# Kernel optimization log

Measured on AMD Instinct MI355X. Metric: run time of the kernel, lower is better.

## Reference

```python
import jax, jax.numpy as jnp
import numpy as np

EPS = 1e-5

def _ln(x, g, b):
    mu = x.mean(-1, keepdims=True)
    var = ((x - mu) ** 2).mean(-1, keepdims=True)
    return (x - mu) * jax.lax.rsqrt(var + EPS) * g + b

def setup_inputs() -> dict:
    B, K, D, H, T = 64, 64, 128, 128, 4
    key = jax.random.key(0)
    ks = jax.random.split(key, 20)
    s = 0.02
    inp = {
        "slots": jax.random.normal(ks[0], (B, K, D), jnp.float32),
        "edge_probs": jax.random.uniform(ks[1], (B, K, K), jnp.float32),
        "edge_types": jax.random.uniform(ks[2], (B, K, K, T), jnp.float32),
        # f_self: LayerNorm(D) -> Linear(D,H) -> ReLU -> Linear(H,D)
        "ls_g": jnp.ones((D,), jnp.float32),
        "ls_b": jnp.zeros((D,), jnp.float32),
        "ws1": jax.random.normal(ks[3], (D, H), jnp.float32) * s,
        "bs1": jnp.zeros((H,), jnp.float32),
        "ws2": jax.random.normal(ks[4], (H, D), jnp.float32) * s,
        "bs2": jnp.zeros((D,), jnp.float32),
        # f_inter[tau]: Linear(2D,H) -> ReLU -> Linear(H,H) -> ReLU -> Linear(H,D), stacked over T
        "wi1": jax.random.normal(ks[5], (T, 2 * D, H), jnp.float32) * s,
        "bi1": jnp.zeros((T, H), jnp.float32),
        "wi2": jax.random.normal(ks[6], (T, H, H), jnp.float32) * s,
        "bi2": jnp.zeros((T, H), jnp.float32),
        "wi3": jax.random.normal(ks[7], (T, H, D), jnp.float32) * s,
        "bi3": jnp.zeros((T, D), jnp.float32),
        # update_mlp: LayerNorm(2D) -> Linear(2D,H) -> ReLU -> Linear(H,D)
        "lu_g": jnp.ones((2 * D,), jnp.float32),
        "lu_b": jnp.zeros((2 * D,), jnp.float32),
        "wu1": jax.random.normal(ks[8], (2 * D, H), jnp.float32) * s,
        "bu1": jnp.zeros((H,), jnp.float32),
        "wu2": jax.random.normal(ks[9], (H, D), jnp.float32) * s,
        "bu2": jnp.zeros((D,), jnp.float32),
    }
    return inp

NUM_MP = 2

def reference(slots, edge_probs, edge_types, ls_g, ls_b, ws1, bs1, ws2, bs2,
              wi1, bi1, wi2, bi2, wi3, bi3, lu_g, lu_b, wu1, bu1, wu2, bu2):
    B, K, D = slots.shape
    T = edge_types.shape[-1]
    h = slots
    for _ in range(NUM_MP):
        # f_self
        delta_self = jax.nn.relu(_ln(h, ls_g, ls_b) @ ws1 + bs1) @ ws2 + bs2
        # all-pairs features: cat[b,i,j] = [h[b,i] (sender), h[b,j] (receiver)]
        sender = jnp.broadcast_to(h[:, :, None, :], (B, K, K, D))
        receiver = jnp.broadcast_to(h[:, None, :, :], (B, K, K, D))
        pair = jnp.concatenate([sender, receiver], axis=-1)  # [B,K,K,2D]
        delta_inter = jnp.zeros_like(h)
        for tau in range(T):
            x = jax.nn.relu(pair @ wi1[tau] + bi1[tau])
            x = jax.nn.relu(x @ wi2[tau] + bi2[tau])
            eff = x @ wi3[tau] + bi3[tau]  # [B,K,K,D]
            w = edge_probs[..., None] * edge_types[..., tau, None]  # [B,K,K,1]
            delta_inter = delta_inter + (eff * w).sum(axis=1)  # sum over sender i
        combined = jnp.concatenate([h + delta_self, delta_inter], axis=-1)
        update = jax.nn.relu(_ln(combined, lu_g, lu_b) @ wu1 + bu1) @ wu2 + bu2
        h = h + update  # residual=True
    return h
```

## Files before the change

### kernel.cpp

```cpp
#include <hip/hip_runtime.h>
#include <hip/hip_fp16.h>

#define BATCH 64
#define KSLOT 64
#define DDIM  128
#define HDIM  128
#define TTYPE 4
#define NSLOT (BATCH*KSLOT)
#define EPSLN 1e-5f
#define YROW  544

typedef _Float16 v8h __attribute__((ext_vector_type(8)));
typedef float    v4f __attribute__((ext_vector_type(4)));

__device__ __forceinline__ float waveAllSum(float v) {
    #pragma unroll
    for (int m = 1; m < 64; m <<= 1) v += __shfl_xor(v, m, 64);
    return v;
}

__global__ __launch_bounds__(256) void k_wconv(
        const float* __restrict__ ws1, const float* __restrict__ wi1,
        const float* __restrict__ ws2, const float* __restrict__ wu1,
        const float* __restrict__ wu2, const float* __restrict__ wi3,
        const float* __restrict__ wi2, const float* __restrict__ bi1,
        const float* __restrict__ bi3,
        __half* __restrict__ ws1T, __half* __restrict__ wi1catT,
        __half* __restrict__ ws2T, __half* __restrict__ wu1T,
        __half* __restrict__ wu2T, __half* __restrict__ w3catT,
        __half* __restrict__ w2T16, float* __restrict__ biascat) {
    __shared__ __align__(16) float tile[128*132];
    int bx = blockIdx.x, tid = threadIdx.x;
    if (bx == 21) {
        for (int idx = tid; idx < 128*32; idx += 256) {
            int o = idx >> 5, c = idx & 31;
            w3catT[(size_t)o*YROW + 512 + c] = (c < 4) ? __float2half(bi3[c*DDIM + o]) : __float2half(0.f);
        }
        for (int idx = tid; idx < 1024; idx += 256) {
            int th = idx >> 7, o = idx & 127;
            biascat[idx] = (th & 1) ? bi1[(th>>1)*HDIM + o] : 0.f;
        }
        return;
    }
    const float* src; __half* dst; int dstride = 128, dcol = 0;
    if (bx == 0)      { src = ws1; dst = ws1T; }
    else if (bx <= 8) { int th = bx-1, tau = th>>1, half = th&1;
                        src = wi1 + ((size_t)tau*256 + half*128)*128;
                        dst = wi1catT + (size_t)th*128*128; }
    else if (bx == 9) { src = ws2; dst = ws2T; }
    else if (bx ==10) { src = wu2; dst = wu2T; }
    else if (bx <=12) { int hh = bx-11; src = wu1 + (size_t)hh*128*128;
                        dst = wu1T; dstride = 256; dcol = hh*128; }
    else if (bx <=16) { int tau = bx-13; src = wi3 + (size_t)tau*16384;
                        dst = w3catT; dstride = YROW; dcol = tau*128; }
    else              { int tau = bx-17; src = wi2 + (size_t)tau*16384;
                        dst = w2T16 + (size_t)tau*16384; }
    for (int idx = tid; idx < 4096; idx += 256) {
        int r = idx >> 5, c4 = idx & 31;
        *(float4*)&tile[r*132 + c4*4] = *(const float4*)&src[(size_t)r*128 + c4*4];
    }
    __syncthreads();
    for (int idx = tid; idx < 8192; idx += 256) {
        int n = idx >> 6, kp = idx & 63;
        __half2 p = __floats2half2_rn(tile[(2*kp)*132 + n], tile[(2*kp+1)*132 + n]);
        *(__half2*)&dst[(size_t)n*dstride + dcol + 2*kp] = p;
    }
}

__global__ __launch_bounds__(256) void k_front(
        const float* __restrict__ h,
        const __half* __restrict__ wi1catT, const float* __restrict__ biascat,
        const float* __restrict__ ls_g, const float* __restrict__ ls_b,
        const __half* __restrict__ ws1T, const float* __restrict__ bs1,
        const __half* __restrict__ ws2T, const float* __restrict__ bs2,
        __half* __restrict__ AtCt, float* __restrict__ comb128) {
    __shared__ __align__(16) char smem[17152];
    int tid = threadIdx.x, lane = tid & 63, w = tid >> 6;
    int n = lane & 15, quad = lane >> 4;
    int row0 = blockIdx.x*16, nb = blockIdx.y;
    if (nb < 4) {
        _Float16* Ha = (_Float16*)smem;
        for (int u = tid; u < 16*32; u += 256) {
            int r = u >> 5, c4 = (u & 31)*4;
            float4 f = *(const float4*)&h[(size_t)(row0 + r)*128 + c4];
            *(__half2*)&Ha[r*136 + c4]     = __floats2half2_rn(f.x, f.y);
            *(__half2*)&Ha[r*136 + c4 + 2] = __floats2half2_rn(f.z, f.w);
        }
        __syncthreads();
        v8h bfrag[4][4];
        #pragma unroll
        for (int ot = 0; ot < 4; ot++) {
            int col = nb*256 + w*64 + ot*16 + n;
            #pragma unroll
            for (int ks = 0; ks < 4; ks++)
                bfrag[ot][ks] = *(const v8h*)&wi1catT[(size_t)col*128 + ks*32 + quad*8];
        }
        v4f acc[4];
        #pragma unroll
        for (int ot = 0; ot < 4; ot++) {
            float b0 = biascat[nb*256 + w*64 + ot*16 + n];
            acc[ot] = (v4f){b0, b0, b0, b0};
        }
        #pragma unroll
        for (int ks = 0; ks < 4; ks++) {
            v8h a = *(const v8h*)&Ha[n*136 + ks*32 + quad*8];
            #pragma unroll
            for (int ot = 0; ot < 4; ot++)
                acc[ot] = __builtin_amdgcn_mfma_f32_16x16x32_f16(a, bfrag[ot][ks], acc[ot], 0, 0, 0);
        }
        #pragma unroll
        for (int ot = 0; ot < 4; ot++)
            #pragma unroll
            for (int r = 0; r < 4; r++) {
                int row = row0 + quad*4 + r, col = nb*256 + w*64 + ot*16 + n;
                AtCt[(size_t)row*1024 + col] = __float2half(acc[ot][r]);
            }
    } else {
        float*    Hrow = (float*)smem;
        _Float16* Xa = (_Float16*)(smem + 8448);
        _Float16* Tt = (_Float16*)(smem + 8448 + 4352);
        v8h b1[2][4], b2[2][4];
        #pragma unroll
        for (int ot = 0; ot < 2; ot++) {
            int col = w*32 + ot*16 + n;
            #pragma unroll
            for (int ks = 0; ks < 4; ks++) {
                b1[ot][ks] = *(const v8h*)&ws1T[(size_t)col*128 + ks*32 + quad*8];
                b2[ot][ks] = *(const v8h*)&ws2T[(size_t)col*128 + ks*32 + quad*8];
            }
        }
        for (int u = tid; u < 16*32; u += 256) {
            int r = u >> 5, c4 = (u & 31)*4;
            *(float4*)&Hrow[r*132 + c4] = *(const float4*)&h[(size_t)(row0 + r)*128 + c4];
        }
        __syncthreads();
        #pragma unroll
        for (int rr = 0; rr < 4; rr++) {
            int r = w*4 + rr;
            float x0 = Hrow[r*132 + 2*lane], x1 = Hrow[r*132 + 2*lane + 1];
            float mu = waveAllSum(x0 + x1) * (1.f/128.f);
            float d0 = x0 - mu, d1 = x1 - mu;
            float var = waveAllSum(d0*d0 + d1*d1) * (1.f/128.f);
            float rs = rsqrtf(var + EPSLN);
            float2 gv = *(const float2*)&ls_g[2*lane];
            float2 bv = *(const float2*)&ls_b[2*lane];
            *(__half2*)&Xa[r*136 + 2*lane] = __floats2half2_rn(d0*rs*gv.x + bv.x, d1*rs*gv.y + bv.y);
        }
        __syncthreads();
        v4f acc[2];
        #pragma unroll
        for (int ot = 0; ot < 2; ot++) { float b0 = bs1[w*32 + ot*16 + n]; acc[ot] = (v4f){b0,b0,b0,b0}; }
        #pragma unroll
        for (int ks = 0; ks < 4; ks++) {
            v8h a = *(const v8h*)&Xa[n*136 + ks*32 + quad*8];
            #pragma unroll
            for (int ot = 0; ot < 2; ot++)
                acc[ot] = __builtin_amdgcn_mfma_f32_16x16x32_f16(a, b1[ot][ks], acc[ot], 0, 0, 0);
        }
        #pragma unroll
        for (int ot = 0; ot < 2; ot++)
            #pragma unroll
            for (int r = 0; r < 4; r++)
                Tt[(quad*4 + r)*136 + w*32 + ot*16 + n] = (_Float16)fmaxf(acc[ot][r], 0.f);
        __syncthreads();
        #pragma unroll
        for (int ot = 0; ot < 2; ot++) { float b0 = bs2[w*32 + ot*16 + n]; acc[ot] = (v4f){b0,b0,b0,b0}; }
        #pragma unroll
        for (int ks = 0; ks < 4; ks++) {
            v8h a = *(const v8h*)&Tt[n*136 + ks*32 + quad*8];
            #pragma unroll
            for (int ot = 0; ot < 2; ot++)
                acc[ot] = __builtin_amdgcn_mfma_f32_16x16x32_f16(a, b2[ot][ks], acc[ot], 0, 0, 0);
        }
        #pragma unroll
        for (int ot = 0; ot < 2; ot++)
            #pragma unroll
            for (int r = 0; r < 4; r++) {
                int rr = quad*4 + r, col = w*32 + ot*16 + n;
                comb128[(size_t)(row0 + rr)*128 + col] = Hrow[rr*132 + col] + acc[ot][r];
            }
    }
}

#define LROW 136
__global__ __launch_bounds__(512) void k_pair(
        const __half* __restrict__ AtCt,
        const __half* __restrict__ w2T16,
        const float* __restrict__ bi2,
        const float* __restrict__ ep, const float* __restrict__ et,
        __half* __restrict__ Ycat) {
    __shared__ __align__(16) _Float16 w2T[HDIM*LROW];
    __shared__ __align__(16) _Float16 Cs[KSLOT*LROW];
    __shared__ __align__(16) _Float16 As[KSLOT*LROW];
    __shared__ __align__(16) _Float16 wS[KSLOT*KSLOT];
    int bx = blockIdx.x, b = bx >> 2, tau = bx & 3;
    int tid = threadIdx.x, lane = tid & 63, w = tid >> 6;
    int jt = w >> 1, oh = w & 1, quad = lane >> 4, n = lane & 15;

    for (int idx = tid; idx < 2048; idx += 512) {
        int o = idx >> 4, seg = (idx & 15)*8;
        *(v8h*)&w2T[o*LROW + seg] = *(const v8h*)&w2T16[((size_t)tau*128 + o)*128 + seg];
    }
    for (int u = tid; u < 1024; u += 512) {
        int j = u >> 4, seg = (u & 15)*8;
        const __half* rp = AtCt + (size_t)(b*KSLOT + j)*1024 + tau*256 + seg;
        *(v8h*)&As[j*LROW + seg] = *(const v8h*)&rp[0];
        *(v8h*)&Cs[j*LROW + seg] = *(const v8h*)&rp[128];
    }
    {
        const float* epb = ep + (size_t)b*KSLOT*KSLOT;
        const float* etb = et + (size_t)b*KSLOT*KSLOT*TTYPE + tau;
        for (int idx = tid; idx < KSLOT*KSLOT; idx += 512)
            wS[idx] = (_Float16)(epb[idx] * etb[(size_t)idx*TTYPE]);
    }
    __syncthreads();

    v8h bfrag[4][4];
    #pragma unroll
    for (int ot = 0; ot < 4; ot++)
        #pragma unroll
        for (int ks = 0; ks < 4; ks++)
            bfrag[ot][ks] = *(const v8h*)&w2T[(oh*64 + ot*16 + n)*LROW + ks*32 + quad*8];
    v8h cfrag[4];
    #pragma unroll
    for (int ks = 0; ks < 4; ks++)
        cfrag[ks] = *(const v8h*)&Cs[(jt*16 + n)*LROW + ks*32 + quad*8];
    float biasv[4];
    #pragma unroll
    for (int ot = 0; ot < 4; ot++) biasv[ot] = bi2[tau*HDIM + oh*64 + ot*16 + n];

    v4f yacc[4];
    #pragma unroll
    for (int ot = 0; ot < 4; ot++) yacc[ot] = (v4f){0.f,0.f,0.f,0.f};
    float wsacc[4] = {0.f,0.f,0.f,0.f};
    const v8h zero8 = {0,0,0,0,0,0,0,0};

    for (int i = 0; i < KSLOT; ++i) {
        v8h x1[4];
        #pragma unroll
        for (int ks = 0; ks < 4; ks++) {
            v8h a = *(const v8h*)&As[i*LROW + ks*32 + quad*8];
            x1[ks] = __builtin_elementwise_max(a + cfrag[ks], zero8);
        }
        _Float16 wv16[4];
        #pragma unroll
        for (int r = 0; r < 4; r++) wv16[r] = wS[i*KSLOT + jt*16 + quad*4 + r];
        #pragma unroll
        for (int ot = 0; ot < 4; ot++) {
            v4f acc = (v4f){biasv[ot], biasv[ot], biasv[ot], biasv[ot]};
            #pragma unroll
            for (int ks = 0; ks < 4; ks++)
                acc = __builtin_amdgcn_mfma_f32_16x16x32_f16(x1[ks], bfrag[ot][ks], acc, 0, 0, 0);
            #pragma unroll
            for (int r = 0; r < 4; r++)
                yacc[ot][r] = fmaf((float)wv16[r], fmaxf(acc[r], 0.f), yacc[ot][r]);
        }
        #pragma unroll
        for (int r = 0; r < 4; r++) wsacc[r] += (float)wv16[r];
    }

    #pragma unroll
    for (int r = 0; r < 4; r++) {
        int j = jt*16 + quad*4 + r;
        __half* yb = Ycat + (size_t)(b*KSLOT + j)*YROW + tau*128 + oh*64;
        #pragma unroll
        for (int ot = 0; ot < 4; ot++)
            yb[ot*16 + n] = __float2half(yacc[ot][r]);
    }
    if (oh == 0 && n == 0) {
        #pragma unroll
        for (int r = 0; r < 4; r++)
            Ycat[(size_t)(b*KSLOT + jt*16 + quad*4 + r)*YROW + 512 + tau] = __float2half(wsacc[r]);
    }
}

__global__ __launch_bounds__(256) void k_mega(
        const __half* __restrict__ Ycat, const __half* __restrict__ w3catT,
        const float* __restrict__ comb128,
        const float* __restrict__ g, const float* __restrict__ bb,
        const __half* __restrict__ wu1T, const float* __restrict__ bu1,
        const __half* __restrict__ wu2T, const float* __restrict__ bu2,
        const float* __restrict__ h, float* __restrict__ hout) {
    __shared__ __align__(16) _Float16 Ys[16*552];
    __shared__ __align__(16) float    Crow[16*260];
    __shared__ __align__(16) _Float16 Xa[16*264];
    __shared__ __align__(16) _Float16 Ut[16*136];
    int tid = threadIdx.x, lane = tid & 63, w = tid >> 6;
    int n = lane & 15, quad = lane >> 4;
    int row0 = blockIdx.x*16;
    for (int u = tid; u < 1024; u += 256) {
        int r = u >> 6, seg = (u & 63)*8;
        *(v8h*)&Ys[r*552 + seg] = *(const v8h*)&Ycat[(size_t)(row0 + r)*YROW + seg];
    }
    {
        int r = tid >> 2, seg = 512 + (tid & 3)*8;
        if (tid < 64) *(v8h*)&Ys[r*552 + seg] = *(const v8h*)&Ycat[(size_t)(row0 + r)*YROW + seg];
    }
    for (int u = tid; u < 16*32; u += 256) {
        int r = u >> 5, c4 = (u & 31)*4;
        *(float4*)&Crow[r*260 + c4] = *(const float4*)&comb128[(size_t)(row0 + r)*128 + c4];
    }
    __syncthreads();
    {
        v4f acc[2];
        acc[0] = (v4f){0.f,0.f,0.f,0.f};
        acc[1] = (v4f){0.f,0.f,0.f,0.f};
        #pragma unroll
        for (int ks = 0; ks < 17; ks++) {
            v8h a = *(const v8h*)&Ys[n*552 + ks*32 + quad*8];
            #pragma unroll
            for (int o2 = 0; o2 < 2; o2++) {
                v8h bfr = *(const v8h*)&w3catT[(size_t)(w*32 + o2*16 + n)*YROW + ks*32 + quad*8];
                acc[o2] = __builtin_amdgcn_mfma_f32_16x16x32_f16(a, bfr, acc[o2], 0, 0, 0);
            }
        }
        #pragma unroll
        for (int o2 = 0; o2 < 2; o2++)
            #pragma unroll
            for (int r = 0; r < 4; r++)
                Crow[(quad*4 + r)*260 + 128 + w*32 + o2*16 + n] = acc[o2][r];
    }
    __syncthreads();
    #pragma unroll
    for (int rr = 0; rr < 4; rr++) {
        int r = w*4 + rr;
        float4 v = *(const float4*)&Crow[r*260 + 4*lane];
        float mu = waveAllSum(v.x + v.y + v.z + v.w) * (1.f/256.f);
        float d0 = v.x-mu, d1 = v.y-mu, d2 = v.z-mu, d3 = v.w-mu;
        float var = waveAllSum(d0*d0 + d1*d1 + d2*d2 + d3*d3) * (1.f/256.f);
        float rs = rsqrtf(var + EPSLN);
        float4 gv = *(const float4*)&g[4*lane];
        float4 bv = *(const float4*)&bb[4*lane];
        *(__half2*)&Xa[r*264 + 4*lane]     = __floats2half2_rn(d0*rs*gv.x + bv.x, d1*rs*gv.y + bv.y);
        *(__half2*)&Xa[r*264 + 4*lane + 2] = __floats2half2_rn(d2*rs*gv.z + bv.z, d3*rs*gv.w + bv.w);
    }
    __syncthreads();
    v4f acc[2];
    #pragma unroll
    for (int ot = 0; ot < 2; ot++) { float b0 = bu1[w*32 + ot*16 + n]; acc[ot] = (v4f){b0,b0,b0,b0}; }
    #pragma unroll
    for (int ks = 0; ks < 8; ks++) {
        v8h a = *(const v8h*)&Xa[n*264 + ks*32 + quad*8];
        #pragma unroll
        for (int ot = 0; ot < 2; ot++) {
            v8h bfr = *(const v8h*)&wu1T[(size_t)(w*32 + ot*16 + n)*256 + ks*32 + quad*8];
            acc[ot] = __builtin_amdgcn_mfma_f32_16x16x32_f16(a, bfr, acc[ot], 0, 0, 0);
        }
    }
    #pragma unroll
    for (int ot = 0; ot < 2; ot++)
        #pragma unroll
        for (int r = 0; r < 4; r++)
            Ut[(quad*4 + r)*136 + w*32 + ot*16 + n] = (_Float16)fmaxf(acc[ot][r], 0.f);
    __syncthreads();
    #pragma unroll
    for (int ot = 0; ot < 2; ot++) { float b0 = bu2[w*32 + ot*16 + n]; acc[ot] = (v4f){b0,b0,b0,b0}; }
    #pragma unroll
    for (int ks = 0; ks < 4; ks++) {
        v8h a = *(const v8h*)&Ut[n*136 + ks*32 + quad*8];
        #pragma unroll
        for (int ot = 0; ot < 2; ot++) {
            v8h bfr = *(const v8h*)&wu2T[(size_t)(w*32 + ot*16 + n)*128 + ks*32 + quad*8];
            acc[ot] = __builtin_amdgcn_mfma_f32_16x16x32_f16(a, bfr, acc[ot], 0, 0, 0);
        }
    }
    #pragma unroll
    for (int ot = 0; ot < 2; ot++)
        #pragma unroll
        for (int r = 0; r < 4; r++) {
            int rr = quad*4 + r, col = w*32 + ot*16 + n;
            hout[(size_t)(row0 + rr)*128 + col] = h[(size_t)(row0 + rr)*128 + col] + acc[ot][r];
        }
}

extern "C" void kernel_launch(void* const* d_in, const int* in_sizes, int n_in,
                              void* d_out, int out_size, void* d_ws, size_t ws_size,
                              hipStream_t stream) {
    const float* slots = (const float*)d_in[0];
    const float* ep    = (const float*)d_in[1];
    const float* et    = (const float*)d_in[2];
    const float* ls_g  = (const float*)d_in[3];
    const float* ls_b  = (const float*)d_in[4];
    const float* ws1   = (const float*)d_in[5];
    const float* bs1   = (const float*)d_in[6];
    const float* ws2   = (const float*)d_in[7];
    const float* bs2   = (const float*)d_in[8];
    const float* wi1   = (const float*)d_in[9];
    const float* bi1   = (const float*)d_in[10];
    const float* wi2   = (const float*)d_in[11];
    const float* bi2   = (const float*)d_in[12];
    const float* wi3   = (const float*)d_in[13];
    const float* bi3   = (const float*)d_in[14];
    const float* lu_g  = (const float*)d_in[15];
    const float* lu_b  = (const float*)d_in[16];
    const float* wu1   = (const float*)d_in[17];
    const float* bu1   = (const float*)d_in[18];
    const float* wu2   = (const float*)d_in[19];
    const float* bu2   = (const float*)d_in[20];
    float* out = (float*)d_out;

    char* p = (char*)d_ws;
    float*  h_buf   = (float*)p;   p += (size_t)NSLOT*DDIM*4;
    __half* AtCt    = (__half*)p;  p += (size_t)NSLOT*1024*2;
    __half* Ycat    = (__half*)p;  p += (size_t)NSLOT*YROW*2;
    float*  comb128 = (float*)p;   p += (size_t)NSLOT*128*4;
    __half* ws1T    = (__half*)p;  p += 128*128*2;
    __half* wi1catT = (__half*)p;  p += 1024*128*2;
    __half* ws2T    = (__half*)p;  p += 128*128*2;
    __half* wu1T    = (__half*)p;  p += 128*256*2;
    __half* wu2T    = (__half*)p;  p += 128*128*2;
    __half* w3catT  = (__half*)p;  p += 128*YROW*2;
    __half* w2T16   = (__half*)p;  p += 4*128*128*2;
    float*  biascat = (float*)p;   p += 1024*4;

    k_wconv<<<22, 256, 0, stream>>>(ws1, wi1, ws2, wu1, wu2, wi3, wi2, bi1, bi3,
                                    ws1T, wi1catT, ws2T, wu1T, wu2T, w3catT, w2T16, biascat);

    for (int mp = 0; mp < 2; mp++) {
        const float* h = (mp == 0) ? slots : h_buf;
        float* hout = (mp == 0) ? h_buf : out;
        k_front<<<dim3(256, 5), 256, 0, stream>>>(h, wi1catT, biascat, ls_g, ls_b,
                                                  ws1T, bs1, ws2T, bs2, AtCt, comb128);
        k_pair<<<BATCH*TTYPE, 512, 0, stream>>>(AtCt, w2T16, bi2, ep, et, Ycat);
        k_mega<<<NSLOT/16, 256, 0, stream>>>(Ycat, w3catT, comb128, lu_g, lu_b,
                                             wu1T, bu1, wu2T, bu2, h, hout);
    }
}
```

Baseline: 229.3 us.

## Double wave count in pair and mega kernels, prefetch next sender row

k_pair now runs 1024 threads per block, with each wave owning 32 output columns instead of 64. This halves the per-wave B fragments and accumulators, and the inner loop software-prefetches the next sender row and edge weights from LDS. k_mega moves to 512 threads, each wave producing 16 output columns, so more waves hide the global weight loads. The trade is more redundant A-operand LDS reads and x1 recomputation per block. Occupancy is also limited by the 1024-thread blocks and LDS use.

New measurement: 252.2 us. 1.1x slower.

```diff
diff --git a/kernel.cpp b/kernel.cpp
--- a/kernel.cpp
+++ b/kernel.cpp
@@ -11,6 +11,7 @@
 #define YROW  544
 
 typedef _Float16 v8h __attribute__((ext_vector_type(8)));
+typedef _Float16 v4h __attribute__((ext_vector_type(4)));
 typedef float    v4f __attribute__((ext_vector_type(4)));
 
 __device__ __forceinline__ float waveAllSum(float v) {
@@ -183,7 +184,7 @@
 }
 
 #define LROW 136
-__global__ __launch_bounds__(512) void k_pair(
+__global__ __launch_bounds__(1024, 4) void k_pair(
         const __half* __restrict__ AtCt,
         const __half* __restrict__ w2T16,
         const float* __restrict__ bi2,
@@ -195,14 +196,14 @@
     __shared__ __align__(16) _Float16 wS[KSLOT*KSLOT];
     int bx = blockIdx.x, b = bx >> 2, tau = bx & 3;
     int tid = threadIdx.x, lane = tid & 63, w = tid >> 6;
-    int jt = w >> 1, oh = w & 1, quad = lane >> 4, n = lane & 15;
-
-    for (int idx = tid; idx < 2048; idx += 512) {
+    int jt = w >> 2, oq = w & 3, quad = lane >> 4, n = lane & 15;
+
+    for (int idx = tid; idx < 2048; idx += 1024) {
         int o = idx >> 4, seg = (idx & 15)*8;
         *(v8h*)&w2T[o*LROW + seg] = *(const v8h*)&w2T16[((size_t)tau*128 + o)*128 + seg];
     }
-    for (int u = tid; u < 1024; u += 512) {
-        int j = u >> 4, seg = (u & 15)*8;
+    {
+        int j = tid >> 4, seg = (tid & 15)*8;
         const __half* rp = AtCt + (size_t)(b*KSLOT + j)*1024 + tau*256 + seg;
         *(v8h*)&As[j*LROW + seg] = *(const v8h*)&rp[0];
         *(v8h*)&Cs[j*LROW + seg] = *(const v8h*)&rp[128];
@@ -210,71 +211,80 @@
     {
         const float* epb = ep + (size_t)b*KSLOT*KSLOT;
         const float* etb = et + (size_t)b*KSLOT*KSLOT*TTYPE + tau;
-        for (int idx = tid; idx < KSLOT*KSLOT; idx += 512)
+        for (int idx = tid; idx < KSLOT*KSLOT; idx += 1024)
             wS[idx] = (_Float16)(epb[idx] * etb[(size_t)idx*TTYPE]);
     }
     __syncthreads();
 
-    v8h bfrag[4][4];
-    #pragma unroll
-    for (int ot = 0; ot < 4; ot++)
+    v8h bfrag[2][4];
+    #pragma unroll
+    for (int ot = 0; ot < 2; ot++)
         #pragma unroll
         for (int ks = 0; ks < 4; ks++)
-            bfrag[ot][ks] = *(const v8h*)&w2T[(oh*64 + ot*16 + n)*LROW + ks*32 + quad*8];
+            bfrag[ot][ks] = *(const v8h*)&w2T[(oq*32 + ot*16 + n)*LROW + ks*32 + quad*8];
     v8h cfrag[4];
     #pragma unroll
     for (int ks = 0; ks < 4; ks++)
         cfrag[ks] = *(const v8h*)&Cs[(jt*16 + n)*LROW + ks*32 + quad*8];
-    float biasv[4];
-    #pragma unroll
-    for (int ot = 0; ot < 4; ot++) biasv[ot] = bi2[tau*HDIM + oh*64 + ot*16 + n];
-
-    v4f yacc[4];
-    #pragma unroll
-    for (int ot = 0; ot < 4; ot++) yacc[ot] = (v4f){0.f,0.f,0.f,0.f};
+    float biasv[2];
+    #pragma unroll
+    for (int ot = 0; ot < 2; ot++) biasv[ot] = bi2[tau*HDIM + oq*32 + ot*16 + n];
+
+    v4f yacc[2];
+    yacc[0] = (v4f){0.f,0.f,0.f,0.f};
+    yacc[1] = (v4f){0.f,0.f,0.f,0.f};
     float wsacc[4] = {0.f,0.f,0.f,0.f};
     const v8h zero8 = {0,0,0,0,0,0,0,0};
 
+    v8h aN[4]; v4h wvN;
+    #pragma unroll
+    for (int ks = 0; ks < 4; ks++) aN[ks] = *(const v8h*)&As[ks*32 + quad*8];
+    wvN = *(const v4h*)&wS[jt*16 + quad*4];
+
     for (int i = 0; i < KSLOT; ++i) {
+        v8h a[4]; v4h wv = wvN;
+        #pragma unroll
+        for (int ks = 0; ks < 4; ks++) a[ks] = aN[ks];
+        if (i < KSLOT-1) {
+            #pragma unroll
+            for (int ks = 0; ks < 4; ks++)
+                aN[ks] = *(const v8h*)&As[(i+1)*LROW + ks*32 + quad*8];
+            wvN = *(const v4h*)&wS[(i+1)*KSLOT + jt*16 + quad*4];
+        }
         v8h x1[4];
         #pragma unroll
-        for (int ks = 0; ks < 4; ks++) {
-            v8h a = *(const v8h*)&As[i*LROW + ks*32 + quad*8];
-            x1[ks] = __builtin_elementwise_max(a + cfrag[ks], zero8);
-        }
-        _Float16 wv16[4];
-        #pragma unroll
-        for (int r = 0; r < 4; r++) wv16[r] = wS[i*KSLOT + jt*16 + quad*4 + r];
-        #pragma unroll
-        for (int ot = 0; ot < 4; ot++) {
+        for (int ks = 0; ks < 4; ks++)
+            x1[ks] = __builtin_elementwise_max(a[ks] + cfrag[ks], zero8);
+        #pragma unroll
+        for (int ot = 0; ot < 2; ot++) {
             v4f acc = (v4f){biasv[ot], biasv[ot], biasv[ot], biasv[ot]};
             #pragma unroll
             for (int ks = 0; ks < 4; ks++)
                 acc = __builtin_amdgcn_mfma_f32_16x16x32_f16(x1[ks], bfrag[ot][ks], acc, 0, 0, 0);
             #pragma unroll
             for (int r = 0; r < 4; r++)
-                yacc[ot][r] = fmaf((float)wv16[r], fmaxf(acc[r], 0.f), yacc[ot][r]);
-        }
-        #pragma unroll
-        for (int r = 0; r < 4; r++) wsacc[r] += (float)wv16[r];
+                yacc[ot][r] = fmaf((float)wv[r], fmaxf(acc[r], 0.f), yacc[ot][r]);
+        }
+        #pragma unroll
+        for (int r = 0; r < 4; r++) wsacc[r] += (float)wv[r];
     }
 
     #pragma unroll
     for (int r = 0; r < 4; r++) {
         int j = jt*16 + quad*4 + r;
-        __half* yb = Ycat + (size_t)(b*KSLOT + j)*YROW + tau*128 + oh*64;
-        #pragma unroll
-        for (int ot = 0; ot < 4; ot++)
+        __half* yb = Ycat + (size_t)(b*KSLOT + j)*YROW + tau*128 + oq*32;
+        #pragma unroll
+        for (int ot = 0; ot < 2; ot++)
             yb[ot*16 + n] = __float2half(yacc[ot][r]);
     }
-    if (oh == 0 && n == 0) {
+    if (oq == 0 && n == 0) {
         #pragma unroll
         for (int r = 0; r < 4; r++)
             Ycat[(size_t)(b*KSLOT + jt*16 + quad*4 + r)*YROW + 512 + tau] = __float2half(wsacc[r]);
     }
 }
 
-__global__ __launch_bounds__(256) void k_mega(
+__global__ __launch_bounds__(512) void k_mega(
         const __half* __restrict__ Ycat, const __half* __restrict__ w3catT,
         const float* __restrict__ comb128,
         const float* __restrict__ g, const float* __restrict__ bb,
@@ -288,42 +298,35 @@
     int tid = threadIdx.x, lane = tid & 63, w = tid >> 6;
     int n = lane & 15, quad = lane >> 4;
     int row0 = blockIdx.x*16;
-    for (int u = tid; u < 1024; u += 256) {
+    for (int u = tid; u < 1024; u += 512) {
         int r = u >> 6, seg = (u & 63)*8;
         *(v8h*)&Ys[r*552 + seg] = *(const v8h*)&Ycat[(size_t)(row0 + r)*YROW + seg];
     }
+    if (tid < 64) {
+        int r = tid >> 2, seg = 512 + (tid & 3)*8;
+        *(v8h*)&Ys[r*552 + seg] = *(const v8h*)&Ycat[(size_t)(row0 + r)*YROW + seg];
+    }
+    if (tid < 512) {
+        int r = tid >> 5, c4 = (tid & 31)*4;
+        *(float4*)&Crow[r*260 + c4] = *(const float4*)&comb128[(size_t)(row0 + r)*128 + c4];
+    }
+    __syncthreads();
     {
-        int r = tid >> 2, seg = 512 + (tid & 3)*8;
-        if (tid < 64) *(v8h*)&Ys[r*552 + seg] = *(const v8h*)&Ycat[(size_t)(row0 + r)*YROW + seg];
-    }
-    for (int u = tid; u < 16*32; u += 256) {
-        int r = u >> 5, c4 = (u & 31)*4;
-        *(float4*)&Crow[r*260 + c4] = *(const float4*)&comb128[(size_t)(row0 + r)*128 + c4];
-    }
-    __syncthreads();
-    {
-        v4f acc[2];
-        acc[0] = (v4f){0.f,0.f,0.f,0.f};
-        acc[1] = (v4f){0.f,0.f,0.f,0.f};
+        v4f acc = (v4f){0.f,0.f,0.f,0.f};
         #pragma unroll
         for (int ks = 0; ks < 17; ks++) {
             v8h a = *(const v8h*)&Ys[n*552 + ks*32 + quad*8];
-            #pragma unroll
-            for (int o2 = 0; o2 < 2; o2++) {
-                v8h bfr = *(const v8h*)&w3catT[(size_t)(w*32 + o2*16 + n)*YROW + ks*32 + quad*8];
-                acc[o2] = __builtin_amdgcn_mfma_f32_16x16x32_f16(a, bfr, acc[o2], 0, 0, 0);
-            }
-        }
-        #pragma unroll
-        for (int o2 = 0; o2 < 2; o2++)
-            #pragma unroll
-            for (int r = 0; r < 4; r++)
-                Crow[(quad*4 + r)*260 + 128 + w*32 + o2*16 + n] = acc[o2][r];
-    }
-    __syncthreads();
-    #pragma unroll
-    for (int rr = 0; rr < 4; rr++) {
-        int r = w*4 + rr;
+            v8h bfr = *(const v8h*)&w3catT[(size_t)(w*16 + n)*YROW + ks*32 + quad*8];
+            acc = __builtin_amdgcn_mfma_f32_16x16x32_f16(a, bfr, acc, 0, 0, 0);
+        }
+        #pragma unroll
+        for (int r = 0; r < 4; r++)
+            Crow[(quad*4 + r)*260 + 128 + w*16 + n] = acc[r];
+    }
+    __syncthreads();
+    #pragma unroll
+    for (int rr = 0; rr < 2; rr++) {
+        int r = w*2 + rr;
         float4 v = *(const float4*)&Crow[r*260 + 4*lane];
         float mu = waveAllSum(v.x + v.y + v.z + v.w) * (1.f/256.f);
         float d0 = v.x-mu, d1 = v.y-mu, d2 = v.z-mu, d3 = v.w-mu;
@@ -335,42 +338,35 @@
         *(__half2*)&Xa[r*264 + 4*lane + 2] = __floats2half2_rn(d2*rs*gv.z + bv.z, d3*rs*gv.w + bv.w);
     }
     __syncthreads();
-    v4f acc[2];
-    #pragma unroll
-    for (int ot = 0; ot < 2; ot++) { float b0 = bu1[w*32 + ot*16 + n]; acc[ot] = (v4f){b0,b0,b0,b0}; }
-    #pragma unroll
-    for (int ks = 0; ks < 8; ks++) {
-        v8h a = *(const v8h*)&Xa[n*264 + ks*32 + quad*8];
-        #pragma unroll
-        for (int ot = 0; ot < 2; ot++) {
-            v8h bfr = *(const v8h*)&wu1T[(size_t)(w*32 + ot*16 + n)*256 + ks*32 + quad*8];
-            acc[ot] = __builtin_amdgcn_mfma_f32_16x16x32_f16(a, bfr, acc[ot], 0, 0, 0);
-        }
-    }
-    #pragma unroll
-    for (int ot = 0; ot < 2; ot++)
+    {
+        float b0 = bu1[w*16 + n];
+        v4f acc = (v4f){b0, b0, b0, b0};
+        #pragma unroll
+        for (int ks = 0; ks < 8; ks++) {
+            v8h a = *(const v8h*)&Xa[n*264 + ks*32 + quad*8];
+            v8h bfr = *(const v8h*)&wu1T[(size_t)(w*16 + n)*256 + ks*32 + quad*8];
+            acc = __builtin_amdgcn_mfma_f32_16x16x32_f16(a, bfr, acc, 0, 0, 0);
+        }
         #pragma unroll
         for (int r = 0; r < 4; r++)
-            Ut[(quad*4 + r)*136 + w*32 + ot*16 + n] = (_Float16)fmaxf(acc[ot][r], 0.f);
-    __syncthreads();
-    #pragma unroll
-    for (int ot = 0; ot < 2; ot++) { float b0 = bu2[w*32 + ot*16 + n]; acc[ot] = (v4f){b0,b0,b0,b0}; }
-    #pragma unroll
-    for (int ks = 0; ks < 4; ks++) {
-        v8h a = *(const v8h*)&Ut[n*136 + ks*32 + quad*8];
-        #pragma unroll
-        for (int ot = 0; ot < 2; ot++) {
-            v8h bfr = *(const v8h*)&wu2T[(size_t)(w*32 + ot*16 + n)*128 + ks*32 + quad*8];
-            acc[ot] = __builtin_amdgcn_mfma_f32_16x16x32_f16(a, bfr, acc[ot], 0, 0, 0);
-        }
-    }
-    #pragma unroll
-    for (int ot = 0; ot < 2; ot++)
+            Ut[(quad*4 + r)*136 + w*16 + n] = (_Float16)fmaxf(acc[r], 0.f);
+    }
+    __syncthreads();
+    {
+        float b0 = bu2[w*16 + n];
+        v4f acc = (v4f){b0, b0, b0, b0};
+        #pragma unroll
+        for (int ks = 0; ks < 4; ks++) {
+            v8h a = *(const v8h*)&Ut[n*136 + ks*32 + quad*8];
+            v8h bfr = *(const v8h*)&wu2T[(size_t)(w*16 + n)*128 + ks*32 + quad*8];
+            acc = __builtin_amdgcn_mfma_f32_16x16x32_f16(a, bfr, acc, 0, 0, 0);
+        }
         #pragma unroll
         for (int r = 0; r < 4; r++) {
-            int rr = quad*4 + r, col = w*32 + ot*16 + n;
-            hout[(size_t)(row0 + rr)*128 + col] = h[(size_t)(row0 + rr)*128 + col] + acc[ot][r];
-        }
+            int rr = quad*4 + r, col = w*16 + n;
+            hout[(size_t)(row0 + rr)*128 + col] = h[(size_t)(row0 + rr)*128 + col] + acc[r];
+        }
+    }
 }
 
 extern "C" void kernel_launch(void* const* d_in, const int* in_sizes, int n_in,
@@ -421,8 +417,8 @@
         float* hout = (mp == 0) ? h_buf : out;
         k_front<<<dim3(256, 5), 256, 0, stream>>>(h, wi1catT, biascat, ls_g, ls_b,
                                                   ws1T, bs1, ws2T, bs2, AtCt, comb128);
-        k_pair<<<BATCH*TTYPE, 512, 0, stream>>>(AtCt, w2T16, bi2, ep, et, Ycat);
-        k_mega<<<NSLOT/16, 256, 0, stream>>>(Ycat, w3catT, comb128, lu_g, lu_b,
+        k_pair<<<BATCH*TTYPE, 1024, 0, stream>>>(AtCt, w2T16, bi2, ep, et, Ycat);
+        k_mega<<<NSLOT/16, 512, 0, stream>>>(Ycat, w3catT, comb128, lu_g, lu_b,
                                              wu1T, bu1, wu2T, bu2, h, hout);
     }
 }
```
